# Optimization experiments

Measured on AMD Instinct MI355X. Metric: run time of the kernel, lower is better.

Reference implementation:

```python
import jax, jax.numpy as jnp
import numpy as np

N, E, H, NH, RBF = 20000, 200000, 128, 8, 64
HD = H // NH
CUT_HI = 5.0


def _ln(t, s, b, eps=1e-6):
    mu = t.mean(-1, keepdims=True)
    var = ((t - mu) ** 2).mean(-1, keepdims=True)
    return (t - mu) * jax.lax.rsqrt(var + eps) * s + b


def _cutoff(w):
    # cosine cutoff, cutoff_lower = 0
    return 0.5 * (jnp.cos(w * (jnp.pi / CUT_HI)) + 1.0) * (w < CUT_HI)


def _xavier(k, fi, fo):
    lim = float(np.sqrt(6.0 / (fi + fo)))
    return jax.random.uniform(k, (fi, fo), minval=-lim, maxval=lim, dtype=jnp.float32)


def setup_inputs() -> dict:
    key = jax.random.key(0)
    ks = jax.random.split(key, 16)
    return {
        "x": jax.random.normal(ks[0], (N, H), jnp.float32),
        "vec": jax.random.normal(ks[1], (N, 3, H), jnp.float32),
        "edge_weight": jax.random.uniform(ks[2], (E, 1), jnp.float32) * 6.0,
        "edge_attr": jax.random.uniform(ks[3], (E, RBF), jnp.float32),
        "edge_vec": jax.random.normal(ks[4], (E, 3), jnp.float32),
        "senders": jax.random.randint(ks[5], (E,), 0, N, jnp.int32),
        "receivers": jax.random.randint(ks[6], (E,), 0, N, jnp.int32),
        "ln_s": jnp.ones((H,), jnp.float32), "ln_b": jnp.zeros((H,), jnp.float32),
        "Wq": _xavier(ks[7], H, H), "bq": jnp.zeros((H,), jnp.float32),
        "Wk": _xavier(ks[8], H, H), "bk": jnp.zeros((H,), jnp.float32),
        "Wv": _xavier(ks[9], H, 3 * H), "bv": jnp.zeros((3 * H,), jnp.float32),
        "Wvec": _xavier(ks[10], H, 3 * H),
        "Wdk": _xavier(ks[11], RBF, H), "bdk": jnp.zeros((H,), jnp.float32),
        "Wdv": _xavier(ks[12], RBF, 3 * H), "bdv": jnp.zeros((3 * H,), jnp.float32),
        "Wo": _xavier(ks[13], H, 3 * H), "bo": jnp.zeros((3 * H,), jnp.float32),
        "qln_s": jnp.ones((HD,), jnp.float32), "qln_b": jnp.zeros((HD,), jnp.float32),
        "kln_s": jnp.ones((HD,), jnp.float32), "kln_b": jnp.zeros((HD,), jnp.float32),
    }


def reference(x, vec, edge_weight, edge_attr, edge_vec, senders, receivers,
              ln_s, ln_b, Wq, bq, Wk, bk, Wv, bv, Wvec, Wdk, bdk, Wdv, bdv,
              Wo, bo, qln_s, qln_b, kln_s, kln_b):
    act = jax.nn.silu
    n = x.shape[0]
    xn = _ln(x, ln_s, ln_b)                                    # [N,H]
    q = _ln((xn @ Wq + bq).reshape(n, NH, HD), qln_s, qln_b)   # [N,h,d]
    k = _ln((xn @ Wk + bk).reshape(n, NH, HD), kln_s, kln_b)   # [N,h,d]
    v = (xn @ Wv + bv).reshape(n, NH, 3 * HD)                  # [N,h,3d]
    vp = vec @ Wvec                                            # [N,3,3H]
    vec1, vec2, vec3 = jnp.split(vp, 3, axis=-1)               # [N,3,H] each
    vec_dot = (vec1 * vec2).sum(axis=1)                        # [N,H]
    vec_h = vec.reshape(n, 3, NH, HD)                          # [N,3,h,d]
    dk = act(edge_attr @ Wdk + bdk).reshape(-1, NH, HD)        # [E,h,d]
    dv = act(edge_attr @ Wdv + bdv).reshape(-1, NH, 3 * HD)    # [E,h,3d]
    # message
    attn = (q[receivers] * k[senders] * dk).sum(axis=-1)       # [E,h]
    attn = act(attn) * _cutoff(edge_weight)                    # [E,h]
    v_j = v[senders] * dv                                      # [E,h,3d]
    xm, m1, m2 = jnp.split(v_j, 3, axis=2)                     # [E,h,d]
    xm = xm * attn[:, :, None]                                 # [E,h,d]
    vec_m = vec_h[senders] * m1[:, None] + m2[:, None] * edge_vec[:, :, None, None]  # [E,3,h,d]
    # aggregate
    x_agg = jax.ops.segment_sum(xm, receivers, num_segments=n).reshape(n, H)
    vec_agg = jax.ops.segment_sum(vec_m, receivers, num_segments=n).reshape(n, 3, H)
    o1, o2, o3 = jnp.split(x_agg @ Wo + bo, 3, axis=1)         # [N,H] each
    dvec = vec3 * o1[:, None] + vec_agg                        # [N,3,H]
    dx = vec_dot * o2 + o3                                     # [N,H]
    return (dx, dvec)
```

## Files before the change

kernel.cpp:

```cpp
#include <hip/hip_runtime.h>
#include <stdint.h>

#define NN 20000
#define NE 200000

typedef __attribute__((ext_vector_type(8))) short bf16x8;
typedef __attribute__((ext_vector_type(4))) float f32x4;

__device__ __forceinline__ float bf2f(uint32_t u) {
  union { uint32_t i; float f; } v; v.i = u << 16; return v.f;
}
__device__ __forceinline__ uint16_t f2bf(float f) {
  union { float f; uint32_t i; } v; v.f = f;
  return (uint16_t)((v.i + 0x7fffu + ((v.i >> 16) & 1u)) >> 16);
}
__device__ __forceinline__ uint32_t pk2(float lo, float hi) {
  return (uint32_t)f2bf(lo) | ((uint32_t)f2bf(hi) << 16);
}
__device__ __forceinline__ float siluf(float x) { return x / (1.f + __expf(-x)); }
__device__ __forceinline__ float prod2(uint32_t q2, uint32_t k2, uint32_t d2) {
  return bf2f(q2 & 0xffffu) * bf2f(k2 & 0xffffu) * bf2f(d2 & 0xffffu)
       + bf2f(q2 >> 16) * bf2f(k2 >> 16) * bf2f(d2 >> 16);
}

__global__ void k_prep(const float* __restrict__ Wq, const float* __restrict__ Wk,
                       const float* __restrict__ Wv, const float* __restrict__ Wvec,
                       const float* __restrict__ Wdk, const float* __restrict__ Wdv,
                       const float* __restrict__ Wo, const float* __restrict__ bq,
                       const float* __restrict__ bk, const float* __restrict__ bv,
                       const float* __restrict__ bdk, const float* __restrict__ bdv,
                       uint16_t* __restrict__ WTqkv, uint16_t* __restrict__ WTvec,
                       uint16_t* __restrict__ WTdkv2, uint16_t* __restrict__ WTo,
                       float* __restrict__ Bqkv, float* __restrict__ Bdkv2) {
  int idx = blockIdx.x * 256 + threadIdx.x;
  if (idx < 98304) {
    int rr = idx >> 7, k = idx & 127;
    float v;
    if (rr < 128)      v = Wq[k * 128 + rr];
    else if (rr < 256) v = Wk[k * 128 + rr - 128];
    else {
      int j2 = rr - 256, j = j2 >> 2, c = j2 & 3;
      v = (c < 3) ? Wv[k * 384 + (j >> 4) * 48 + c * 16 + (j & 15)] : 0.f;
    }
    WTqkv[idx] = f2bf(v);
    return;
  }
  idx -= 98304;
  if (idx < 49152) {
    int c = idx >> 7, k = idx & 127;
    WTvec[idx] = f2bf(Wvec[k * 384 + c]);
    return;
  }
  idx -= 49152;
  if (idx < 32768) {
    int rr = idx >> 6, k = idx & 63;
    float v;
    if (rr < 128) v = Wdk[k * 128 + rr];
    else {
      int j = rr - 128, p = j >> 7, hd = j & 127;
      v = Wdv[k * 384 + (hd >> 4) * 48 + p * 16 + (hd & 15)];
    }
    WTdkv2[idx] = f2bf(v);
    return;
  }
  idx -= 32768;
  if (idx < 49152) {
    int c = idx >> 7, k = idx & 127;
    WTo[idx] = f2bf(Wo[k * 384 + c]);
    return;
  }
  idx -= 49152;
  if (idx < 768) {
    if (idx < 128)      Bqkv[idx] = bq[idx];
    else if (idx < 256) Bqkv[idx] = bk[idx - 128];
    else {
      int j2 = idx - 256, j = j2 >> 2, c = j2 & 3;
      Bqkv[idx] = (c < 3) ? bv[(j >> 4) * 48 + c * 16 + (j & 15)] : 0.f;
    }
  } else if (idx < 1280) {
    int t = idx - 768;
    if (t < 128) Bdkv2[t] = bdk[t];
    else {
      int j = t - 128, p = j >> 7, hd = j & 127;
      Bdkv2[t] = bdv[(hd >> 4) * 48 + p * 16 + (hd & 15)];
    }
  }
}

__global__ void k_node_pre(const float* __restrict__ x, const float* __restrict__ s,
                           const float* __restrict__ b, const float* __restrict__ vec,
                           uint16_t* __restrict__ xn_b, uint16_t* __restrict__ combo) {
  if (blockIdx.x < 5000) {
    int gt = blockIdx.x * 256 + threadIdx.x;
    int node = gt >> 6, lane = gt & 63;
    if (node >= NN) return;
    const float* row = x + (size_t)node * 128;
    float2 v = *(const float2*)&row[lane * 2];
    float sum = v.x + v.y, sq = v.x * v.x + v.y * v.y;
    #pragma unroll
    for (int off = 32; off; off >>= 1) { sum += __shfl_xor(sum, off); sq += __shfl_xor(sq, off); }
    float mu = sum * (1.f / 128.f);
    float var = sq * (1.f / 128.f) - mu * mu;
    float rs = rsqrtf(var + 1e-6f);
    float o0 = (v.x - mu) * rs * s[lane * 2] + b[lane * 2];
    float o1 = (v.y - mu) * rs * s[lane * 2 + 1] + b[lane * 2 + 1];
    ((uint32_t*)xn_b)[(size_t)node * 64 + lane] = pk2(o0, o1);
  } else {
    int i = (blockIdx.x - 5000) * 256 + threadIdx.x;
    if (i >= NN * 128) return;
    int n = i >> 7, j = i & 127;
    const float* vr = vec + (size_t)n * 384 + j;
    uint16_t* cb = &combo[(size_t)n * 768 + j * 6];
    cb[3] = f2bf(vr[0]);
    *(uint32_t*)&cb[4] = pk2(vr[128], vr[256]);
  }
}

__global__ void k_hist(const int* __restrict__ rcv, int* __restrict__ deg) {
  int e = blockIdx.x * 256 + threadIdx.x;
  if (e < NE) atomicAdd(&deg[rcv[e]], 1);
}

__global__ void k_scan1(const int* __restrict__ deg, int* __restrict__ bsum) {
  __shared__ int ws[4];
  int i = blockIdx.x * 256 + threadIdx.x;
  int x = (i < NN) ? deg[i] : 0;
  #pragma unroll
  for (int d = 32; d; d >>= 1) x += __shfl_xor(x, d);
  if ((threadIdx.x & 63) == 0) ws[threadIdx.x >> 6] = x;
  __syncthreads();
  if (threadIdx.x == 0) bsum[blockIdx.x] = ws[0] + ws[1] + ws[2] + ws[3];
}

__global__ void k_scan2(int* __restrict__ bsum, int nb, int* __restrict__ off) {
  int lane = threadIdx.x;
  int carry = 0;
  for (int base = 0; base < nb; base += 64) {
    int i = base + lane;
    int x = (i < nb) ? bsum[i] : 0;
    int v = x;
    #pragma unroll
    for (int d = 1; d < 64; d <<= 1) { int y = __shfl_up(v, d); if (lane >= d) v += y; }
    if (i < nb) bsum[i] = carry + v - x;
    carry += __shfl(v, 63);
  }
  if (lane == 0) off[NN] = carry;
}

__global__ void k_scan3(const int* __restrict__ deg, const int* __restrict__ bsum,
                        int* __restrict__ off, int* __restrict__ cur) {
  __shared__ int ws[4];
  int t = threadIdx.x, lane = t & 63, w = t >> 6;
  int i = blockIdx.x * 256 + t;
  int x = (i < NN) ? deg[i] : 0;
  int v = x;
  #pragma unroll
  for (int d = 1; d < 64; d <<= 1) { int y = __shfl_up(v, d); if (lane >= d) v += y; }
  if (lane == 63) ws[w] = v;
  __syncthreads();
  int wadd = 0;
  for (int j = 0; j < w; j++) wadd += ws[j];
  int excl = bsum[blockIdx.x] + wadd + v - x;
  if (i < NN) { off[i] = excl; cur[i] = excl; }
}

__global__ void k_scatter(const int* __restrict__ rcv, int* __restrict__ cur,
                          int* __restrict__ perm) {
  int e = blockIdx.x * 256 + threadIdx.x;
  if (e >= NE) return;
  int pos = atomicAdd(&cur[rcv[e]], 1);
  perm[pos] = e;
}

__global__ void k_permute(const float* __restrict__ ea, const int* __restrict__ perm,
                          const int* __restrict__ snd, const int* __restrict__ rcv,
                          const float* __restrict__ ew, const float* __restrict__ evec,
                          uint16_t* __restrict__ ea_perm, int* __restrict__ sndp,
                          int* __restrict__ rcvp, float4* __restrict__ edata) {
  int idx = blockIdx.x * 256 + threadIdx.x;
  if (idx >= NE * 16) return;
  int i = idx >> 4, j = idx & 15;
  int e = perm[i];
  float4 v = *(const float4*)&ea[(size_t)e * 64 + j * 4];
  uint2 o;
  o.x = pk2(v.x, v.y);
  o.y = pk2(v.z, v.w);
  *(uint2*)&ea_perm[(size_t)i * 64 + j * 4] = o;
  if (j == 0) {
    sndp[i] = snd[e];
    rcvp[i] = rcv[e];
    float w = ew[e];
    float cut = (w < 5.f) ? 0.5f * (__cosf(w * 0.628318530717958648f) + 1.f) : 0.f;
    edata[i] = make_float4(evec[e * 3], evec[e * 3 + 1], evec[e * 3 + 2], cut);
  }
}

template <int KTOT, bool OUT_BF16, bool SILU, bool AF32>
__global__ __launch_bounds__(256) void k_gemm(const void* __restrict__ A,
                                              const uint16_t* __restrict__ BT,
                                              const float* __restrict__ bias,
                                              void* __restrict__ Cout, int M, int Fo) {
  __shared__ __align__(16) uint16_t As[128 * 72];
  __shared__ __align__(16) uint16_t Bs[128 * 72];
  const uint16_t* A16 = (const uint16_t*)A;
  const float* A32 = (const float*)A;
  int t = threadIdx.x;
  int l = t & 63;
  int row0 = blockIdx.y * 128, col0 = blockIdx.x * 128;
  int wm = ((t >> 6) >> 1) * 64, wn = ((t >> 6) & 1) * 64;
  f32x4 acc[4][4] = {};
  for (int kt = 0; kt < KTOT; kt += 64) {
    __syncthreads();
    #pragma unroll
    for (int i = 0; i < 4; i++) {
      int c = i * 256 + t;
      int row = c >> 3, ko = (c & 7) * 8;
      uint4 av = make_uint4(0u, 0u, 0u, 0u);
      int gr = row0 + row;
      if (gr < M) {
        if (AF32) {
          float4 f0 = *(const float4*)&A32[(size_t)gr * KTOT + kt + ko];
          float4 f1 = *(const float4*)&A32[(size_t)gr * KTOT + kt + ko + 4];
          av = make_uint4(pk2(f0.x, f0.y), pk2(f0.z, f0.w), pk2(f1.x, f1.y), pk2(f1.z, f1.w));
        } else {
          av = *(const uint4*)&A16[(size_t)gr * KTOT + kt + ko];
        }
      }
      *(uint4*)&As[row * 72 + ko] = av;
      uint4 bw = *(const uint4*)&BT[(size_t)(col0 + row) * KTOT + kt + ko];
      *(uint4*)&Bs[row * 72 + ko] = bw;
    }
    __syncthreads();
    #pragma unroll
    for (int kk = 0; kk < 64; kk += 32) {
      bf16x8 af[4], bfr[4];
      #pragma unroll
      for (int mf = 0; mf < 4; mf++)
        af[mf] = *(const bf16x8*)&As[(wm + mf * 16 + (l & 15)) * 72 + (l >> 4) * 8 + kk];
      #pragma unroll
      for (int nf = 0; nf < 4; nf++)
        bfr[nf] = *(const bf16x8*)&Bs[(wn + nf * 16 + (l & 15)) * 72 + (l >> 4) * 8 + kk];
      #pragma unroll
      for (int mf = 0; mf < 4; mf++)
        #pragma unroll
        for (int nf = 0; nf < 4; nf++)
          acc[mf][nf] = __builtin_amdgcn_mfma_f32_16x16x32_bf16(af[mf], bfr[nf], acc[mf][nf], 0, 0, 0);
    }
  }
  float* Cf = (float*)Cout;
  uint16_t* Cb = (uint16_t*)Cout;
  #pragma unroll
  for (int mf = 0; mf < 4; mf++) {
    #pragma unroll
    for (int r = 0; r < 4; r++) {
      int grow = row0 + wm + mf * 16 + (l >> 4) * 4 + r;
      if (grow >= M) continue;
      #pragma unroll
      for (int nf = 0; nf < 4; nf++) {
        int gcol = col0 + wn + nf * 16 + (l & 15);
        float v = acc[mf][nf][r];
        if (bias) v += bias[gcol];
        if (SILU) v = siluf(v);
        if (OUT_BF16) Cb[(size_t)grow * Fo + gcol] = f2bf(v);
        else          Cf[(size_t)grow * Fo + gcol] = v;
      }
    }
  }
}

__global__ __launch_bounds__(256) void k_gemm_qkv(
    const uint16_t* __restrict__ A, const uint16_t* __restrict__ BT,
    const float* __restrict__ bias, const float* __restrict__ qs,
    const float* __restrict__ qb, const float* __restrict__ ks,
    const float* __restrict__ kb, uint16_t* __restrict__ qk_b,
    uint16_t* __restrict__ combo) {
  __shared__ __align__(16) uint16_t As[128 * 72];
  __shared__ __align__(16) uint16_t Bs[128 * 72];
  int t = threadIdx.x;
  int l = t & 63;
  int row0 = blockIdx.y * 128, col0 = blockIdx.x * 128;
  int wm = ((t >> 6) >> 1) * 64, wn = ((t >> 6) & 1) * 64;
  f32x4 acc[4][4] = {};
  for (int kt = 0; kt < 128; kt += 64) {
    __syncthreads();
    #pragma unroll
    for (int i = 0; i < 4; i++) {
      int c = i * 256 + t;
      int row = c >> 3, ko = (c & 7) * 8;
      uint4 av = make_uint4(0u, 0u, 0u, 0u);
      int gr = row0 + row;
      if (gr < NN) av = *(const uint4*)&A[(size_t)gr * 128 + kt + ko];
      *(uint4*)&As[row * 72 + ko] = av;
      uint4 bw = *(const uint4*)&BT[(size_t)(col0 + row) * 128 + kt + ko];
      *(uint4*)&Bs[row * 72 + ko] = bw;
    }
    __syncthreads();
    #pragma unroll
    for (int kk = 0; kk < 64; kk += 32) {
      bf16x8 af[4], bfr[4];
      #pragma unroll
      for (int mf = 0; mf < 4; mf++)
        af[mf] = *(const bf16x8*)&As[(wm + mf * 16 + (l & 15)) * 72 + (l >> 4) * 8 + kk];
      #pragma unroll
      for (int nf = 0; nf < 4; nf++)
        bfr[nf] = *(const bf16x8*)&Bs[(wn + nf * 16 + (l & 15)) * 72 + (l >> 4) * 8 + kk];
      #pragma unroll
      for (int mf = 0; mf < 4; mf++)
        #pragma unroll
        for (int nf = 0; nf < 4; nf++)
          acc[mf][nf] = __builtin_amdgcn_mfma_f32_16x16x32_bf16(af[mf], bfr[nf], acc[mf][nf], 0, 0, 0);
    }
  }
  int d = l & 15;
  if (col0 < 256) {
    float sc_q = qs[d], bb_q = qb[d], sc_k = ks[d], bb_k = kb[d];
    #pragma unroll
    for (int mf = 0; mf < 4; mf++) {
      #pragma unroll
      for (int r = 0; r < 4; r++) {
        int grow = row0 + wm + mf * 16 + (l >> 4) * 4 + r;
        bool ok = grow < NN;
        #pragma unroll
        for (int nf = 0; nf < 4; nf++) {
          int gcol = col0 + wn + nf * 16 + d;
          float v = acc[mf][nf][r] + bias[gcol];
          float s1 = v;
          s1 += __shfl_xor(s1, 1); s1 += __shfl_xor(s1, 2);
          s1 += __shfl_xor(s1, 4); s1 += __shfl_xor(s1, 8);
          float mu = s1 * (1.f / 16.f);
          float dd = v - mu;
          float s2 = dd * dd;
          s2 += __shfl_xor(s2, 1); s2 += __shfl_xor(s2, 2);
          s2 += __shfl_xor(s2, 4); s2 += __shfl_xor(s2, 8);
          float rs = rsqrtf(s2 * (1.f / 16.f) + 1e-6f);
          bool isq = gcol < 128;
          float ov = dd * rs * (isq ? sc_q : sc_k) + (isq ? bb_q : bb_k);
          if (ok) qk_b[(size_t)grow * 256 + gcol] = f2bf(ov);
        }
      }
    }
  } else {
    #pragma unroll
    for (int mf = 0; mf < 4; mf++) {
      #pragma unroll
      for (int r = 0; r < 4; r++) {
        int grow = row0 + wm + mf * 16 + (l >> 4) * 4 + r;
        if (grow >= NN) continue;
        #pragma unroll
        for (int nf = 0; nf < 4; nf++) {
          int gcol = col0 + wn + nf * 16 + d;
          int j2 = gcol - 256, j = j2 >> 2, c = j2 & 3;
          if (c < 3)
            combo[(size_t)grow * 768 + j * 6 + c] = f2bf(acc[mf][nf][r] + bias[gcol]);
        }
      }
    }
  }
}

__device__ __forceinline__ void o_pass(const float* __restrict__ A32,
                                       const uint16_t* __restrict__ BT, int row0, int cb,
                                       int t, int l, int wm, int wn,
                                       uint16_t* As, uint16_t* Bs, f32x4 (&acc)[4][4]) {
  for (int kt = 0; kt < 128; kt += 64) {
    __syncthreads();
    #pragma unroll
    for (int i = 0; i < 4; i++) {
      int c = i * 256 + t;
      int row = c >> 3, ko = (c & 7) * 8;
      uint4 av = make_uint4(0u, 0u, 0u, 0u);
      int gr = row0 + row;
      if (gr < NN) {
        float4 f0 = *(const float4*)&A32[(size_t)gr * 128 + kt + ko];
        float4 f1 = *(const float4*)&A32[(size_t)gr * 128 + kt + ko + 4];
        av = make_uint4(pk2(f0.x, f0.y), pk2(f0.z, f0.w), pk2(f1.x, f1.y), pk2(f1.z, f1.w));
      }
      *(uint4*)&As[row * 72 + ko] = av;
      uint4 bw = *(const uint4*)&BT[(size_t)(cb * 128 + row) * 128 + kt + ko];
      *(uint4*)&Bs[row * 72 + ko] = bw;
    }
    __syncthreads();
    #pragma unroll
    for (int kk = 0; kk < 64; kk += 32) {
      bf16x8 af[4], bfr[4];
      #pragma unroll
      for (int mf = 0; mf < 4; mf++)
        af[mf] = *(const bf16x8*)&As[(wm + mf * 16 + (l & 15)) * 72 + (l >> 4) * 8 + kk];
      #pragma unroll
      for (int nf = 0; nf < 4; nf++)
        bfr[nf] = *(const bf16x8*)&Bs[(wn + nf * 16 + (l & 15)) * 72 + (l >> 4) * 8 + kk];
      #pragma unroll
      for (int mf = 0; mf < 4; mf++)
        #pragma unroll
        for (int nf = 0; nf < 4; nf++)
          acc[mf][nf] = __builtin_amdgcn_mfma_f32_16x16x32_bf16(af[mf], bfr[nf], acc[mf][nf], 0, 0, 0);
    }
  }
}

__global__ __launch_bounds__(256) void k_gemm_o(
    const uint16_t* __restrict__ BT, const float* __restrict__ bo,
    const uint16_t* __restrict__ vp, float* __restrict__ dout) {
  __shared__ __align__(16) uint16_t As[128 * 72];
  __shared__ __align__(16) uint16_t Bs[128 * 72];
  float* xagg = dout;
  float* vecagg = dout + (size_t)NN * 128;
  int t = threadIdx.x;
  int l = t & 63;
  int row0 = blockIdx.y * 128;
  int wm = ((t >> 6) >> 1) * 64, wn = ((t >> 6) & 1) * 64;
  f32x4 acc0[4][4] = {}, acc1[4][4] = {}, acc2[4][4] = {};
  o_pass(xagg, BT, row0, 0, t, l, wm, wn, As, Bs, acc0);
  o_pass(xagg, BT, row0, 1, t, l, wm, wn, As, Bs, acc1);
  o_pass(xagg, BT, row0, 2, t, l, wm, wn, As, Bs, acc2);
  int d = l & 15;
  #pragma unroll
  for (int mf = 0; mf < 4; mf++) {
    #pragma unroll
    for (int r = 0; r < 4; r++) {
      int grow = row0 + wm + mf * 16 + (l >> 4) * 4 + r;
      if (grow >= NN) continue;
      const uint16_t* vpn = vp + (size_t)grow * 1152;
      #pragma unroll
      for (int nf = 0; nf < 4; nf++) {
        int col = wn + nf * 16 + d;
        float o1 = acc0[mf][nf][r] + bo[col];
        float o2 = acc1[mf][nf][r] + bo[128 + col];
        float o3 = acc2[mf][nf][r] + bo[256 + col];
        float vd = 0.f;
        #pragma unroll
        for (int c = 0; c < 3; c++)
          vd += bf2f(vpn[c * 384 + col]) * bf2f(vpn[c * 384 + 128 + col]);
        xagg[(size_t)grow * 128 + col] = vd * o2 + o3;
        #pragma unroll
        for (int c = 0; c < 3; c++) {
          size_t vi = ((size_t)grow * 3 + c) * 128 + col;
          vecagg[vi] = bf2f(vpn[c * 384 + 256 + col]) * o1 + vecagg[vi];
        }
      }
    }
  }
}

#define MTS 516

__device__ __forceinline__ void mfma32(const uint16_t* As, int r0,
                                       const uint16_t* __restrict__ BT2, int cb,
                                       int wn, int l, f32x4 acc[2][2]) {
  #pragma unroll
  for (int kk = 0; kk < 2; kk++) {
    bf16x8 af[2];
    #pragma unroll
    for (int mf = 0; mf < 2; mf++)
      af[mf] = *(const bf16x8*)&As[(r0 + mf * 16 + (l & 15)) * 68 + (l >> 4) * 8 + kk * 32];
    #pragma unroll
    for (int nf = 0; nf < 2; nf++) {
      bf16x8 bv = *(const bf16x8*)&BT2[(size_t)(cb * 128 + wn + nf * 16 + (l & 15)) * 64 +
                                       (l >> 4) * 8 + kk * 32];
      #pragma unroll
      for (int mf = 0; mf < 2; mf++)
        acc[mf][nf] = __builtin_amdgcn_mfma_f32_16x16x32_bf16(af[mf], bv, acc[mf][nf], 0, 0, 0);
    }
  }
}

__device__ __forceinline__ void silu_slot(uint16_t* mt, const float bsv[2], int slot,
                                          int wn, int l, f32x4 acc[2][2]) {
  #pragma unroll
  for (int mf = 0; mf < 2; mf++)
    #pragma unroll
    for (int r = 0; r < 4; r++) {
      int row = mf * 16 + (l >> 4) * 4 + r;
      #pragma unroll
      for (int nf = 0; nf < 2; nf++) {
        int c = wn + nf * 16 + (l & 15);
        mt[row * MTS + c * 4 + slot] = f2bf(siluf(acc[mf][nf][r] + bsv[nf]));
      }
    }
}

__device__ __forceinline__ void silu_dk(uint16_t* mtd, const float bsv[2],
                                        int wn, int l, f32x4 acc[2][2]) {
  #pragma unroll
  for (int mf = 0; mf < 2; mf++)
    #pragma unroll
    for (int r = 0; r < 4; r++) {
      int row = mf * 16 + (l >> 4) * 4 + r;
      #pragma unroll
      for (int nf = 0; nf < 2; nf++) {
        int c = wn + nf * 16 + (l & 15);
        mtd[row * 140 + c] = f2bf(siluf(acc[mf][nf][r] + bsv[nf]));
      }
    }
}

__global__ __launch_bounds__(256) void k_edge_all(
    const uint16_t* __restrict__ eap, const int* __restrict__ sndp,
    const int* __restrict__ rcvp, const int* __restrict__ off,
    const float4* __restrict__ edata, const uint16_t* __restrict__ WT2,
    const float* __restrict__ Bd2, const uint16_t* __restrict__ qk_b,
    const uint16_t* __restrict__ combo, float* __restrict__ xagg,
    float* __restrict__ vecagg) {
  __shared__ __align__(16) uint16_t As[64 * 68];
  __shared__ __align__(16) uint16_t mt[32 * MTS];
  __shared__ __align__(16) uint16_t mtd[32 * 140];
  __shared__ float attn_l[32 * 8];
  __shared__ int sndl[64], rcvl[64], lo_g[64], hi_g[64];
  __shared__ float4 ed4[64];

  int e0 = blockIdx.x * 64;
  int t = threadIdx.x, l = t & 63, wn = (t >> 6) * 32;

  if (t < 64) {
    int e = e0 + t;
    int r = rcvp[e];
    sndl[t] = sndp[e]; rcvl[t] = r;
    lo_g[t] = off[r]; hi_g[t] = off[r + 1];
    ed4[t] = edata[e];
  }
  #pragma unroll
  for (int i = 0; i < 2; i++) {
    int c = i * 256 + t;
    int row = c >> 3, ko = (c & 7) * 8;
    *(uint4*)&As[row * 68 + ko] = *(const uint4*)&eap[(size_t)(e0 + row) * 64 + ko];
  }
  float bs[4][2];
  #pragma unroll
  for (int cb = 0; cb < 4; cb++) {
    bs[cb][0] = Bd2[cb * 128 + wn + (l & 15)];
    bs[cb][1] = Bd2[cb * 128 + wn + 16 + (l & 15)];
  }
  __syncthreads();

  #pragma unroll
  for (int half = 0; half < 2; half++) {
    int r0 = half * 32;
    { f32x4 acc[2][2] = {}; mfma32(As, r0, WT2, 0, wn, l, acc); silu_dk(mtd, bs[0], wn, l, acc); }
    __syncthreads();
    {
      int el = t >> 3, h = t & 7;
      int ge = r0 + el;
      int rn = rcvl[ge], sn = sndl[ge];
      const uint16_t* qb_ = qk_b + (size_t)rn * 256 + h * 16;
      const uint16_t* kb_ = qk_b + (size_t)sn * 256 + 128 + h * 16;
      uint4 q0 = *(const uint4*)qb_;
      uint4 q1 = *(const uint4*)(qb_ + 8);
      uint4 k0 = *(const uint4*)kb_;
      uint4 k1 = *(const uint4*)(kb_ + 8);
      { f32x4 acc[2][2] = {}; mfma32(As, r0, WT2, 1, wn, l, acc); silu_slot(mt, bs[1], 0, wn, l, acc); }
      { f32x4 acc[2][2] = {}; mfma32(As, r0, WT2, 2, wn, l, acc); silu_slot(mt, bs[2], 1, wn, l, acc); }
      { f32x4 acc[2][2] = {}; mfma32(As, r0, WT2, 3, wn, l, acc); silu_slot(mt, bs[3], 2, wn, l, acc); }
      const uint32_t* dp = (const uint32_t*)&mtd[el * 140 + h * 16];
      uint32_t qa[8] = {q0.x, q0.y, q0.z, q0.w, q1.x, q1.y, q1.z, q1.w};
      uint32_t ka[8] = {k0.x, k0.y, k0.z, k0.w, k1.x, k1.y, k1.z, k1.w};
      float dot = 0.f;
      #pragma unroll
      for (int j = 0; j < 8; j++) dot += prod2(qa[j], ka[j], dp[j]);
      attn_l[el * 8 + h] = siluf(dot) * ed4[ge].w;
    }
    __syncthreads();
    {
      int col = t & 127, sub = t >> 7;
      int i0 = r0 + sub * 16, i1 = i0 + 16;
      int ha = col >> 4;
      float accx = 0.f, a0 = 0.f, a1 = 0.f, a2 = 0.f;
      #pragma unroll 8
      for (int i = i0; i < i1; i++) {
        int li = i - r0;
        int n = rcvl[i], s = sndl[i];
        const uint16_t* cp = &combo[(size_t)s * 768 + col * 6];
        uint32_t u0 = *(const uint32_t*)cp;
        uint32_t u1 = *(const uint32_t*)(cp + 2);
        uint32_t u2 = *(const uint32_t*)(cp + 4);
        uint2 mr = *(const uint2*)&mt[li * MTS + col * 4];
        float a = attn_l[li * 8 + ha];
        float xmv = bf2f(mr.x & 0xffffu), m1v = bf2f(mr.x >> 16), m2v = bf2f(mr.y & 0xffffu);
        accx += bf2f(u0 & 0xffffu) * xmv * a;
        float mm1 = bf2f(u0 >> 16) * m1v;
        float mm2 = bf2f(u1 & 0xffffu) * m2v;
        float4 ev = ed4[i];
        a0 += bf2f(u1 >> 16)     * mm1 + ev.x * mm2;
        a1 += bf2f(u2 & 0xffffu) * mm1 + ev.y * mm2;
        a2 += bf2f(u2 >> 16)     * mm1 + ev.z * mm2;
        if (i == i1 - 1 || rcvl[i + 1] != n) {
          bool cont = (lo_g[i] >= e0 + i0) && (hi_g[i] <= e0 + i1);
          float* dx_ = &xagg[(size_t)n * 128 + col];
          float* d0 = &vecagg[((size_t)n * 3 + 0) * 128 + col];
          float* d1 = &vecagg[((size_t)n * 3 + 1) * 128 + col];
          float* d2 = &vecagg[((size_t)n * 3 + 2) * 128 + col];
          if (cont) { *dx_ = accx; *d0 = a0; *d1 = a1; *d2 = a2; }
          else { atomicAdd(dx_, accx); atomicAdd(d0, a0); atomicAdd(d1, a1); atomicAdd(d2, a2); }
          accx = a0 = a1 = a2 = 0.f;
        }
      }
    }
    __syncthreads();
  }
}

static inline int cdiv_i(long long a, long long b) { return (int)((a + b - 1) / b); }

extern "C" void kernel_launch(void* const* d_in, const int* in_sizes, int n_in,
                              void* d_out, int out_size, void* d_ws, size_t ws_size,
                              hipStream_t stream) {
  const float* x    = (const float*)d_in[0];
  const float* vec  = (const float*)d_in[1];
  const float* ew   = (const float*)d_in[2];
  const float* ea   = (const float*)d_in[3];
  const float* evec = (const float*)d_in[4];
  const int*   snd  = (const int*)d_in[5];
  const int*   rcv  = (const int*)d_in[6];
  const float* ln_s = (const float*)d_in[7];
  const float* ln_b = (const float*)d_in[8];
  const float* Wq = (const float*)d_in[9];   const float* bq = (const float*)d_in[10];
  const float* Wk = (const float*)d_in[11];  const float* bk = (const float*)d_in[12];
  const float* Wv = (const float*)d_in[13];  const float* bv = (const float*)d_in[14];
  const float* Wvec = (const float*)d_in[15];
  const float* Wdk = (const float*)d_in[16]; const float* bdk = (const float*)d_in[17];
  const float* Wdv = (const float*)d_in[18]; const float* bdv = (const float*)d_in[19];
  const float* Wo = (const float*)d_in[20];  const float* bo = (const float*)d_in[21];
  const float* qln_s = (const float*)d_in[22]; const float* qln_b = (const float*)d_in[23];
  const float* kln_s = (const float*)d_in[24]; const float* kln_b = (const float*)d_in[25];
  (void)in_sizes; (void)n_in; (void)ws_size;

  uint8_t* p = (uint8_t*)d_ws;
  auto alloc = [&](size_t bytes) -> uint8_t* {
    uint8_t* r = p; p += (bytes + 255) & ~(size_t)255; return r;
  };
  uint16_t* WTqkv = (uint16_t*)alloc(768 * 128 * 2);
  float*    Bqkv  = (float*)alloc(768 * 4);
  uint16_t* WTvec = (uint16_t*)alloc(384 * 128 * 2);
  uint16_t* WTdkv = (uint16_t*)alloc(512 * 64 * 2);
  float*    Bdkv  = (float*)alloc(512 * 4);
  uint16_t* WTo   = (uint16_t*)alloc(384 * 128 * 2);
  int*      deg   = (int*)alloc(NN * 4);
  int*      off   = (int*)alloc((NN + 1) * 4);
  int*      cur   = (int*)alloc(NN * 4);
  int*      bsum  = (int*)alloc(256 * 4);
  int*      perm  = (int*)alloc((size_t)NE * 4);
  int*      sndp  = (int*)alloc((size_t)NE * 4);
  int*      rcvp  = (int*)alloc((size_t)NE * 4);
  float4*   edata = (float4*)alloc((size_t)NE * 16);
  uint16_t* ea_perm = (uint16_t*)alloc((size_t)NE * 64 * 2);
  uint16_t* xn_b  = (uint16_t*)alloc((size_t)NN * 128 * 2);
  uint16_t* combo = (uint16_t*)alloc((size_t)NN * 768 * 2);
  uint16_t* qk_b  = (uint16_t*)alloc((size_t)NN * 256 * 2);
  uint16_t* vp    = (uint16_t*)alloc((size_t)NN * 3 * 384 * 2);

  float* xagg   = (float*)d_out;
  float* vecagg = (float*)d_out + (size_t)NN * 128;

  hipMemsetAsync(d_out, 0, (size_t)out_size * 4, stream);

  k_prep<<<cdiv_i(98304 + 49152 + 32768 + 49152 + 1280, 256), 256, 0, stream>>>(
      Wq, Wk, Wv, Wvec, Wdk, Wdv, Wo, bq, bk, bv, bdk, bdv,
      WTqkv, WTvec, WTdkv, WTo, Bqkv, Bdkv);

  int NSB = cdiv_i(NN, 256);
  hipMemsetAsync(deg, 0, NN * 4, stream);
  k_hist<<<cdiv_i(NE, 256), 256, 0, stream>>>(rcv, deg);
  k_scan1<<<NSB, 256, 0, stream>>>(deg, bsum);
  k_scan2<<<1, 64, 0, stream>>>(bsum, NSB, off);
  k_scan3<<<NSB, 256, 0, stream>>>(deg, bsum, off, cur);
  k_scatter<<<cdiv_i(NE, 256), 256, 0, stream>>>(rcv, cur, perm);
  k_permute<<<cdiv_i((long long)NE * 16, 256), 256, 0, stream>>>(ea, perm, snd, rcv, ew, evec,
                                                                 ea_perm, sndp, rcvp, edata);

  k_node_pre<<<5000 + cdiv_i((long long)NN * 128, 256), 256, 0, stream>>>(
      x, ln_s, ln_b, vec, xn_b, combo);

  { dim3 g(6, cdiv_i(NN, 128));
    k_gemm_qkv<<<g, 256, 0, stream>>>(xn_b, WTqkv, Bqkv, qln_s, qln_b, kln_s, kln_b,
                                      qk_b, combo); }

  { dim3 g(384 / 128, cdiv_i((long long)NN * 3, 128));
    k_gemm<128, true, false, true><<<g, 256, 0, stream>>>(vec, WTvec, nullptr, vp, NN * 3, 384); }

  k_edge_all<<<NE / 64, 256, 0, stream>>>(ea_perm, sndp, rcvp, off, edata, WTdkv, Bdkv,
                                          qk_b, combo, xagg, vecagg);

  { dim3 g(1, cdiv_i(NN, 128));
    k_gemm_o<<<g, 256, 0, stream>>>(WTo, bo, vp, (float*)d_out); }
}
```

Before: 356.2 us.

## Gather edge_attr in edge kernel, fold output zeroing, split head LayerNorm out

The separate permuted bf16 copy of edge_attr is dropped. The edge kernel now gathers fp32 rows through perm and converts them to bf16 while filling shared memory, which removes one full write and read of a 200k×64 buffer. Zeroing of the output moves from hipMemsetAsync into extra blocks of the node pre-pass. The per-head q/k LayerNorm is moved out of the GEMM epilogue into a separate small kernel that reads a raw q/k buffer, adding one launch and an extra round trip for that buffer.

```diff
diff --git a/kernel.cpp b/kernel.cpp
--- a/kernel.cpp
+++ b/kernel.cpp
@@ -89,7 +89,8 @@
 
 __global__ void k_node_pre(const float* __restrict__ x, const float* __restrict__ s,
                            const float* __restrict__ b, const float* __restrict__ vec,
-                           uint16_t* __restrict__ xn_b, uint16_t* __restrict__ combo) {
+                           uint16_t* __restrict__ xn_b, uint16_t* __restrict__ combo,
+                           float4* __restrict__ dz) {
   if (blockIdx.x < 5000) {
     int gt = blockIdx.x * 256 + threadIdx.x;
     int node = gt >> 6, lane = gt & 63;
@@ -105,7 +106,7 @@
     float o0 = (v.x - mu) * rs * s[lane * 2] + b[lane * 2];
     float o1 = (v.y - mu) * rs * s[lane * 2 + 1] + b[lane * 2 + 1];
     ((uint32_t*)xn_b)[(size_t)node * 64 + lane] = pk2(o0, o1);
-  } else {
+  } else if (blockIdx.x < 15000) {
     int i = (blockIdx.x - 5000) * 256 + threadIdx.x;
     if (i >= NN * 128) return;
     int n = i >> 7, j = i & 127;
@@ -113,6 +114,10 @@
     uint16_t* cb = &combo[(size_t)n * 768 + j * 6];
     cb[3] = f2bf(vr[0]);
     *(uint32_t*)&cb[4] = pk2(vr[128], vr[256]);
+  } else {
+    int i = (blockIdx.x - 15000) * 256 + threadIdx.x;
+    if (i >= NN * 128) return;
+    dz[i] = make_float4(0.f, 0.f, 0.f, 0.f);
   }
 }
 
@@ -172,27 +177,18 @@
   perm[pos] = e;
 }
 
-__global__ void k_permute(const float* __restrict__ ea, const int* __restrict__ perm,
-                          const int* __restrict__ snd, const int* __restrict__ rcv,
-                          const float* __restrict__ ew, const float* __restrict__ evec,
-                          uint16_t* __restrict__ ea_perm, int* __restrict__ sndp,
+__global__ void k_permute(const int* __restrict__ perm, const int* __restrict__ snd,
+                          const int* __restrict__ rcv, const float* __restrict__ ew,
+                          const float* __restrict__ evec, int* __restrict__ sndp,
                           int* __restrict__ rcvp, float4* __restrict__ edata) {
-  int idx = blockIdx.x * 256 + threadIdx.x;
-  if (idx >= NE * 16) return;
-  int i = idx >> 4, j = idx & 15;
+  int i = blockIdx.x * 256 + threadIdx.x;
+  if (i >= NE) return;
   int e = perm[i];
-  float4 v = *(const float4*)&ea[(size_t)e * 64 + j * 4];
-  uint2 o;
-  o.x = pk2(v.x, v.y);
-  o.y = pk2(v.z, v.w);
-  *(uint2*)&ea_perm[(size_t)i * 64 + j * 4] = o;
-  if (j == 0) {
-    sndp[i] = snd[e];
-    rcvp[i] = rcv[e];
-    float w = ew[e];
-    float cut = (w < 5.f) ? 0.5f * (__cosf(w * 0.628318530717958648f) + 1.f) : 0.f;
-    edata[i] = make_float4(evec[e * 3], evec[e * 3 + 1], evec[e * 3 + 2], cut);
-  }
+  sndp[i] = snd[e];
+  rcvp[i] = rcv[e];
+  float w = ew[e];
+  float cut = (w < 5.f) ? 0.5f * (__cosf(w * 0.628318530717958648f) + 1.f) : 0.f;
+  edata[i] = make_float4(evec[e * 3], evec[e * 3 + 1], evec[e * 3 + 2], cut);
 }
 
 template <int KTOT, bool OUT_BF16, bool SILU, bool AF32>
@@ -268,11 +264,9 @@
   }
 }
 
-__global__ __launch_bounds__(256) void k_gemm_qkv(
+__global__ __launch_bounds__(256) void k_gemm_qkv2(
     const uint16_t* __restrict__ A, const uint16_t* __restrict__ BT,
-    const float* __restrict__ bias, const float* __restrict__ qs,
-    const float* __restrict__ qb, const float* __restrict__ ks,
-    const float* __restrict__ kb, uint16_t* __restrict__ qk_b,
+    const float* __restrict__ bias, uint16_t* __restrict__ qk_raw,
     uint16_t* __restrict__ combo) {
   __shared__ __align__(16) uint16_t As[128 * 72];
   __shared__ __align__(16) uint16_t Bs[128 * 72];
@@ -312,50 +306,46 @@
     }
   }
   int d = l & 15;
-  if (col0 < 256) {
-    float sc_q = qs[d], bb_q = qb[d], sc_k = ks[d], bb_k = kb[d];
-    #pragma unroll
-    for (int mf = 0; mf < 4; mf++) {
-      #pragma unroll
-      for (int r = 0; r < 4; r++) {
-        int grow = row0 + wm + mf * 16 + (l >> 4) * 4 + r;
-        bool ok = grow < NN;
-        #pragma unroll
-        for (int nf = 0; nf < 4; nf++) {
-          int gcol = col0 + wn + nf * 16 + d;
-          float v = acc[mf][nf][r] + bias[gcol];
-          float s1 = v;
-          s1 += __shfl_xor(s1, 1); s1 += __shfl_xor(s1, 2);
-          s1 += __shfl_xor(s1, 4); s1 += __shfl_xor(s1, 8);
-          float mu = s1 * (1.f / 16.f);
-          float dd = v - mu;
-          float s2 = dd * dd;
-          s2 += __shfl_xor(s2, 1); s2 += __shfl_xor(s2, 2);
-          s2 += __shfl_xor(s2, 4); s2 += __shfl_xor(s2, 8);
-          float rs = rsqrtf(s2 * (1.f / 16.f) + 1e-6f);
-          bool isq = gcol < 128;
-          float ov = dd * rs * (isq ? sc_q : sc_k) + (isq ? bb_q : bb_k);
-          if (ok) qk_b[(size_t)grow * 256 + gcol] = f2bf(ov);
+  #pragma unroll
+  for (int mf = 0; mf < 4; mf++) {
+    #pragma unroll
+    for (int r = 0; r < 4; r++) {
+      int grow = row0 + wm + mf * 16 + (l >> 4) * 4 + r;
+      if (grow >= NN) continue;
+      #pragma unroll
+      for (int nf = 0; nf < 4; nf++) {
+        int gcol = col0 + wn + nf * 16 + d;
+        float v = acc[mf][nf][r] + bias[gcol];
+        if (col0 < 256) {
+          qk_raw[(size_t)grow * 256 + gcol] = f2bf(v);
+        } else {
+          int j2 = gcol - 256, j = j2 >> 2, c = j2 & 3;
+          if (c < 3) combo[(size_t)grow * 768 + j * 6 + c] = f2bf(v);
         }
       }
     }
-  } else {
-    #pragma unroll
-    for (int mf = 0; mf < 4; mf++) {
-      #pragma unroll
-      for (int r = 0; r < 4; r++) {
-        int grow = row0 + wm + mf * 16 + (l >> 4) * 4 + r;
-        if (grow >= NN) continue;
-        #pragma unroll
-        for (int nf = 0; nf < 4; nf++) {
-          int gcol = col0 + wn + nf * 16 + d;
-          int j2 = gcol - 256, j = j2 >> 2, c = j2 & 3;
-          if (c < 3)
-            combo[(size_t)grow * 768 + j * 6 + c] = f2bf(acc[mf][nf][r] + bias[gcol]);
-        }
-      }
-    }
-  }
+  }
+}
+
+__global__ void k_headln(const uint16_t* __restrict__ qkv, const float* __restrict__ qs,
+                         const float* __restrict__ qb, const float* __restrict__ ks,
+                         const float* __restrict__ kb, uint16_t* __restrict__ out) {
+  int idx = blockIdx.x * 256 + threadIdx.x;
+  if (idx >= NN * 16) return;
+  int n = idx >> 4, ph = idx & 15, part = ph >> 3, h = ph & 7;
+  const uint16_t* src = qkv + (size_t)n * 256 + part * 128 + h * 16;
+  float v[16], sum = 0.f;
+  #pragma unroll
+  for (int i = 0; i < 16; i++) { v[i] = bf2f(src[i]); sum += v[i]; }
+  float mu = sum * (1.f / 16.f), var = 0.f;
+  #pragma unroll
+  for (int i = 0; i < 16; i++) { float dd = v[i] - mu; var += dd * dd; }
+  float rs = rsqrtf(var * (1.f / 16.f) + 1e-6f);
+  const float* sc = part ? ks : qs;
+  const float* bb = part ? kb : qb;
+  uint16_t* dst = out + (size_t)n * 256 + part * 128 + h * 16;
+  #pragma unroll
+  for (int i = 0; i < 16; i++) dst[i] = f2bf((v[i] - mu) * rs * sc[i] + bb[i]);
 }
 
 __device__ __forceinline__ void o_pass(const float* __restrict__ A32,
@@ -495,12 +485,12 @@
 }
 
 __global__ __launch_bounds__(256) void k_edge_all(
-    const uint16_t* __restrict__ eap, const int* __restrict__ sndp,
-    const int* __restrict__ rcvp, const int* __restrict__ off,
-    const float4* __restrict__ edata, const uint16_t* __restrict__ WT2,
-    const float* __restrict__ Bd2, const uint16_t* __restrict__ qk_b,
-    const uint16_t* __restrict__ combo, float* __restrict__ xagg,
-    float* __restrict__ vecagg) {
+    const float* __restrict__ ea, const int* __restrict__ perm,
+    const int* __restrict__ sndp, const int* __restrict__ rcvp,
+    const int* __restrict__ off, const float4* __restrict__ edata,
+    const uint16_t* __restrict__ WT2, const float* __restrict__ Bd2,
+    const uint16_t* __restrict__ qk_b, const uint16_t* __restrict__ combo,
+    float* __restrict__ xagg, float* __restrict__ vecagg) {
   __shared__ __align__(16) uint16_t As[64 * 68];
   __shared__ __align__(16) uint16_t mt[32 * MTS];
   __shared__ __align__(16) uint16_t mtd[32 * 140];
@@ -518,11 +508,21 @@
     lo_g[t] = off[r]; hi_g[t] = off[r + 1];
     ed4[t] = edata[e];
   }
-  #pragma unroll
-  for (int i = 0; i < 2; i++) {
-    int c = i * 256 + t;
-    int row = c >> 3, ko = (c & 7) * 8;
-    *(uint4*)&As[row * 68 + ko] = *(const uint4*)&eap[(size_t)(e0 + row) * 64 + ko];
+  {
+    int row = t >> 2, qo = (t & 3) * 16;
+    int pe = perm[e0 + row];
+    const float* src = ea + (size_t)pe * 64 + qo;
+    float4 f0 = *(const float4*)src;
+    float4 f1 = *(const float4*)(src + 4);
+    float4 f2 = *(const float4*)(src + 8);
+    float4 f3 = *(const float4*)(src + 12);
+    uint4 o0, o1;
+    o0.x = pk2(f0.x, f0.y); o0.y = pk2(f0.z, f0.w);
+    o0.z = pk2(f1.x, f1.y); o0.w = pk2(f1.z, f1.w);
+    o1.x = pk2(f2.x, f2.y); o1.y = pk2(f2.z, f2.w);
+    o1.z = pk2(f3.x, f3.y); o1.w = pk2(f3.z, f3.w);
+    *(uint4*)&As[row * 68 + qo] = o0;
+    *(uint4*)&As[row * 68 + qo + 8] = o1;
   }
   float bs[4][2];
   #pragma unroll
@@ -621,7 +621,7 @@
   const float* Wo = (const float*)d_in[20];  const float* bo = (const float*)d_in[21];
   const float* qln_s = (const float*)d_in[22]; const float* qln_b = (const float*)d_in[23];
   const float* kln_s = (const float*)d_in[24]; const float* kln_b = (const float*)d_in[25];
-  (void)in_sizes; (void)n_in; (void)ws_size;
+  (void)in_sizes; (void)n_in; (void)out_size; (void)ws_size;
 
   uint8_t* p = (uint8_t*)d_ws;
   auto alloc = [&](size_t bytes) -> uint8_t* {
@@ -641,16 +641,14 @@
   int*      sndp  = (int*)alloc((size_t)NE * 4);
   int*      rcvp  = (int*)alloc((size_t)NE * 4);
   float4*   edata = (float4*)alloc((size_t)NE * 16);
-  uint16_t* ea_perm = (uint16_t*)alloc((size_t)NE * 64 * 2);
   uint16_t* xn_b  = (uint16_t*)alloc((size_t)NN * 128 * 2);
+  uint16_t* qk_raw = (uint16_t*)alloc((size_t)NN * 256 * 2);
+  uint16_t* qk_b  = (uint16_t*)alloc((size_t)NN * 256 * 2);
   uint16_t* combo = (uint16_t*)alloc((size_t)NN * 768 * 2);
-  uint16_t* qk_b  = (uint16_t*)alloc((size_t)NN * 256 * 2);
   uint16_t* vp    = (uint16_t*)alloc((size_t)NN * 3 * 384 * 2);
 
   float* xagg   = (float*)d_out;
   float* vecagg = (float*)d_out + (size_t)NN * 128;
-
-  hipMemsetAsync(d_out, 0, (size_t)out_size * 4, stream);
 
   k_prep<<<cdiv_i(98304 + 49152 + 32768 + 49152 + 1280, 256), 256, 0, stream>>>(
       Wq, Wk, Wv, Wvec, Wdk, Wdv, Wo, bq, bk, bv, bdk, bdv,
@@ -663,20 +661,19 @@
   k_scan2<<<1, 64, 0, stream>>>(bsum, NSB, off);
   k_scan3<<<NSB, 256, 0, stream>>>(deg, bsum, off, cur);
   k_scatter<<<cdiv_i(NE, 256), 256, 0, stream>>>(rcv, cur, perm);
-  k_permute<<<cdiv_i((long long)NE * 16, 256), 256, 0, stream>>>(ea, perm, snd, rcv, ew, evec,
-                                                                 ea_perm, sndp, rcvp, edata);
-
-  k_node_pre<<<5000 + cdiv_i((long long)NN * 128, 256), 256, 0, stream>>>(
-      x, ln_s, ln_b, vec, xn_b, combo);
+  k_permute<<<cdiv_i(NE, 256), 256, 0, stream>>>(perm, snd, rcv, ew, evec, sndp, rcvp, edata);
+
+  k_node_pre<<<25000, 256, 0, stream>>>(x, ln_s, ln_b, vec, xn_b, combo, (float4*)d_out);
 
   { dim3 g(6, cdiv_i(NN, 128));
-    k_gemm_qkv<<<g, 256, 0, stream>>>(xn_b, WTqkv, Bqkv, qln_s, qln_b, kln_s, kln_b,
-                                      qk_b, combo); }
+    k_gemm_qkv2<<<g, 256, 0, stream>>>(xn_b, WTqkv, Bqkv, qk_raw, combo); }
+  k_headln<<<cdiv_i((long long)NN * 16, 256), 256, 0, stream>>>(qk_raw, qln_s, qln_b,
+                                                               kln_s, kln_b, qk_b);
 
   { dim3 g(384 / 128, cdiv_i((long long)NN * 3, 128));
     k_gemm<128, true, false, true><<<g, 256, 0, stream>>>(vec, WTvec, nullptr, vp, NN * 3, 384); }
 
-  k_edge_all<<<NE / 64, 256, 0, stream>>>(ea_perm, sndp, rcvp, off, edata, WTdkv, Bdkv,
+  k_edge_all<<<NE / 64, 256, 0, stream>>>(ea, perm, sndp, rcvp, off, edata, WTdkv, Bdkv,
                                           qk_b, combo, xagg, vecagg);
 
   { dim3 g(1, cdiv_i(NN, 128));
```

Measured after the change: 338.0 us. 1.05x faster.
